# Kernel tuning notes

Hardware: AMD Instinct MI355X
Metric: run time of the kernel (lower is better)

## Reference

```python
import jax, jax.numpy as jnp
import numpy as np

F, N, E = 8, 2048, 32768          # frames, atoms/frame, directed edges/frame
C, NT, NB, NSH = 32, 4, 8, 4      # channels, atom types, Bessel basis, (lmax+1)^2 for lmax=1
R_MAX, L_BOX, NUM_LAYERS = 6.0, 8.0, 3


def setup_inputs() -> dict:
    key = jax.random.key(0)
    ks = jax.random.split(key, 8)
    pos = jax.random.uniform(ks[0], (F, N, 3), jnp.float32) * L_BOX
    src = jax.random.randint(ks[1], (F, 1, E), 0, N)
    off = jax.random.randint(ks[2], (F, 1, E), 1, N)  # avoid self edges
    edge_index = jnp.concatenate([src, (src + off) % N], axis=1).astype(jnp.int32)
    cell = jnp.full((F, 3), L_BOX, jnp.float32)
    atom_types = jax.random.randint(ks[3], (F, N), 0, NT).astype(jnp.int32)
    W_embed = jax.random.normal(ks[4], (NT, C), jnp.float32) * 0.5
    W_rad = jax.random.normal(ks[5], (NUM_LAYERS, NB, C * NSH), jnp.float32) / np.sqrt(NB)
    W_mix = jax.random.normal(ks[6], (NUM_LAYERS, C, C), jnp.float32) / np.sqrt(C)
    w_out = jax.random.normal(ks[7], (C,), jnp.float32) / np.sqrt(C)
    return dict(pos=pos, edge_index=edge_index, cell=cell, atom_types=atom_types,
                W_embed=W_embed, W_rad=W_rad, W_mix=W_mix, w_out=w_out, cut_off=4)


def _atomic_energy(pos_flat, src, dst, shift, at_flat, W_embed, W_rad, W_mix, w_out):
    # edge vectors with (detached) PBC cell shift
    vec = pos_flat[dst] - pos_flat[src] + shift                      # [Et,3]
    r = jnp.sqrt(jnp.sum(vec * vec, -1) + 1e-12)                     # [Et]
    # spherical harmonics lmax=1, component normalization
    Y = jnp.concatenate([jnp.ones_like(r)[:, None],
                         np.sqrt(3.0) * vec / r[:, None]], axis=1)   # [Et,4]
    # Bessel radial basis with p=6 polynomial cutoff envelope
    x = r / R_MAX
    n = jnp.arange(1, NB + 1, dtype=pos_flat.dtype)
    bessel = np.sqrt(2.0 / R_MAX) * jnp.sin(n[None] * np.pi * x[:, None]) / r[:, None]
    env = (1.0 - 28.0 * x**6 + 48.0 * x**7 - 21.0 * x**8) * (x < 1.0).astype(pos_flat.dtype)
    basis = bessel * env[:, None]                                    # [Et,NB]
    FN = pos_flat.shape[0]
    h0 = jax.nn.one_hot(at_flat, NT, dtype=pos_flat.dtype) @ W_embed  # [FN,C]
    feat = jnp.zeros((FN, C, NSH), pos_flat.dtype).at[:, :, 0].set(h0)
    for l in range(NUM_LAYERS):
        R = (basis @ W_rad[l]).reshape(-1, C, NSH)                   # [Et,C,4]
        # gather scalar src feature, tensor-product with SH, radial weight
        msg = R * feat[src, :, 0][:, :, None] * Y[:, None, :]        # [Et,C,4]
        agg = jax.ops.segment_sum(msg, dst, num_segments=FN)         # scatter
        feat = feat + jnp.einsum('ncK,cd->ndK', agg, W_mix[l])       # resnet
    return feat[:, :, 0] @ w_out                                     # [FN]


def reference(pos, edge_index, cell, atom_types, W_embed, W_rad, W_mix, w_out, cut_off):
    Fn, Nn, Ee = pos.shape[0], pos.shape[1], edge_index.shape[2]
    pos_flat = pos.reshape(-1, 3)
    # offset edge indices per frame, flatten frame-major
    ei = (edge_index + (jnp.arange(Fn, dtype=edge_index.dtype) * Nn)[:, None, None])
    ei = ei.transpose(1, 0, 2).reshape(2, -1)
    src, dst = ei[0], ei[1]
    cell_e = jnp.repeat(cell, Ee, axis=0)                            # [F*E,3]
    co = jnp.asarray(cut_off, pos.dtype)
    v = pos_flat[dst] - pos_flat[src]
    shift = jax.lax.stop_gradient(
        cell_e * ((v < -co).astype(pos.dtype) - (v > co).astype(pos.dtype)))
    # symmetrize edges (both directions)
    src2 = jnp.concatenate([src, dst]); dst2 = jnp.concatenate([dst, src])
    shift2 = jnp.concatenate([shift, -shift], axis=0)
    at_flat = atom_types.reshape(-1)
    e_fn = lambda p: _atomic_energy(p, src2, dst2, shift2, at_flat,
                                    W_embed, W_rad, W_mix, w_out)
    atomic_e = e_fn(pos_flat)                                        # [F*N]
    total_energy = atomic_e.reshape(Fn, Nn).sum(axis=1)              # [F]
    force = -jax.grad(lambda p: e_fn(p).sum())(pos_flat)             # -dE/dpos
    return total_energy, force.reshape(Fn, Nn, 3)
```

## Files before the change

kernel.cpp:

```cpp
#include <hip/hip_runtime.h>
#include <math.h>

#define F_NUM 8
#define N_AT 2048
#define E_EDGE 32768
#define FE (F_NUM*E_EDGE)
#define FN (F_NUM*N_AT)
#define CAP 72
#define PI_F 3.14159265358979f

#if defined(__has_builtin)
#if __has_builtin(__builtin_amdgcn_fdot2)
#define HAS_FDOT2 1
#endif
#endif

typedef _Float16 h2 __attribute__((ext_vector_type(2)));

#define XSWZ(bid, G) (((bid) & 7) * ((G) >> 3) + ((bid) >> 3))

__device__ __forceinline__ unsigned short f2b(float x) {
    unsigned int u = __float_as_uint(x);
    u += 0x8000u;
    return (unsigned short)(u >> 16);
}
__device__ __forceinline__ float blo(unsigned int u) { return __uint_as_float(u << 16); }
__device__ __forceinline__ float bhi(unsigned int u) { return __uint_as_float(u & 0xffff0000u); }
__device__ __forceinline__ float b2f(unsigned short u) { return __uint_as_float((unsigned)u << 16); }

__device__ __forceinline__ unsigned f2h(float x) {
    union { _Float16 h; unsigned short u; } cv;
    cv.h = (_Float16)x;
    return (unsigned)cv.u;
}
__device__ __forceinline__ h2 u2h2(unsigned u) {
    union { unsigned u; h2 h; } cv;
    cv.u = u;
    return cv.h;
}
__device__ __forceinline__ float dot8h(uint4 q, const h2* w) {
#ifdef HAS_FDOT2
    float a = __builtin_amdgcn_fdot2(u2h2(q.x), w[0], 0.f, false);
    a = __builtin_amdgcn_fdot2(u2h2(q.y), w[1], a, false);
    a = __builtin_amdgcn_fdot2(u2h2(q.z), w[2], a, false);
    a = __builtin_amdgcn_fdot2(u2h2(q.w), w[3], a, false);
    return a;
#else
    h2 a0 = u2h2(q.x), a1 = u2h2(q.y), a2 = u2h2(q.z), a3 = u2h2(q.w);
    return (float)a0.x*(float)w[0].x + (float)a0.y*(float)w[0].y
         + (float)a1.x*(float)w[1].x + (float)a1.y*(float)w[1].y
         + (float)a2.x*(float)w[2].x + (float)a2.y*(float)w[2].y
         + (float)a3.x*(float)w[3].x + (float)a3.y*(float)w[3].y;
#endif
}
__device__ __forceinline__ void prep_wr(const float* __restrict__ Wrad_l, int c, h2* wr) {
#pragma unroll
    for (int bb = 0; bb < 4; bb++) {
        h2 t;
        t.x = (_Float16)Wrad_l[(2*bb)   * 128 + c * 4];
        t.y = (_Float16)Wrad_l[(2*bb+1) * 128 + c * 4];
        wr[bb] = t;
    }
}

__global__ __launch_bounds__(256) void k_zg(
    int4* __restrict__ cnt4, const float* __restrict__ w_out,
    const float* __restrict__ Wmix2, float* __restrict__ g2)
{
    int bid = blockIdx.x;
    if (bid < 16) {
        cnt4[bid * 256 + threadIdx.x] = make_int4(0, 0, 0, 0);
    } else if (threadIdx.x < 32) {
        int c = threadIdx.x;
        float acc = 0.f;
#pragma unroll
        for (int d = 0; d < 32; d++) acc += w_out[d] * Wmix2[c * 32 + d];
        g2[c] = acc;
    }
}


__global__ __launch_bounds__(256) void k_edges(
    const float* __restrict__ pos, const int* __restrict__ eidx,
    const float* __restrict__ cell, const int* __restrict__ co_p,
    const int* __restrict__ at,
    uint4* __restrict__ dbq, float4* __restrict__ unit, uint2* __restrict__ ab,
    int* __restrict__ cnt, uint4* __restrict__ rec)
{
    int bid = XSWZ(blockIdx.x, FE / 256);
    int k = bid * 256 + threadIdx.x;
    int f = k >> 15;
    int e = k & (E_EDGE - 1);
    int a = eidx[f * 2 * E_EDGE + e] + f * N_AT;
    int b = eidx[f * 2 * E_EDGE + E_EDGE + e] + f * N_AT;
    int ta = at[a], tb = at[b];
    float co = (float)co_p[0];

    float vec[3];
#pragma unroll
    for (int d = 0; d < 3; d++) {
        float v  = pos[3 * b + d] - pos[3 * a + d];
        float cl = cell[3 * f + d];
        float sh = cl * ((v < -co ? 1.f : 0.f) - (v > co ? 1.f : 0.f));
        vec[d] = v + sh;
    }
    float r2   = vec[0]*vec[0] + vec[1]*vec[1] + vec[2]*vec[2] + 1e-12f;
    float r    = sqrtf(r2);
    float rinv = 1.f / r;
    unit[k] = make_float4(vec[0]*rinv, vec[1]*rinv, vec[2]*rinv, 0.f);
    ab[k] = make_uint2((unsigned)((a << 2) | ta), (unsigned)((b << 2) | tb));

    float x = r * (1.f / 6.f);
    float env = 0.f, denv = 0.f;
    if (x < 1.f) {
        float x2 = x*x, x3 = x2*x, x5 = x2*x3, x6 = x5*x, x7 = x6*x, x8 = x7*x;
        env  = 1.f - 28.f*x6 + 48.f*x7 - 21.f*x8;
        denv = -168.f*x5 + 336.f*x6 - 168.f*x7;
    }
    float s1, c1;
    sincosf(PI_F * x, &s1, &c1);
    float sn = s1, cn = c1;
    const float C0 = 0.57735026919f;
    float bs[8], db[8];
#pragma unroll
    for (int n = 1; n <= 8; n++) {
        float kn  = (float)n * PI_F * (1.f / 6.f);
        float bes = C0 * sn * rinv;
        bs[n-1] = bes * env;
        db[n-1] = C0 * rinv * (kn * cn - sn * rinv) * env + bes * denv * (1.f / 6.f);
        float sn2 = sn * c1 + cn * s1;
        float cn2 = cn * c1 - sn * s1;
        sn = sn2; cn = cn2;
    }
    uint4 B, D;
    B.x = f2h(bs[0]) | (f2h(bs[1]) << 16);
    B.y = f2h(bs[2]) | (f2h(bs[3]) << 16);
    B.z = f2h(bs[4]) | (f2h(bs[5]) << 16);
    B.w = f2h(bs[6]) | (f2h(bs[7]) << 16);
    D.x = f2h(db[0]) | (f2h(db[1]) << 16);
    D.y = f2h(db[2]) | (f2h(db[3]) << 16);
    D.z = f2h(db[4]) | (f2h(db[5]) << 16);
    D.w = f2h(db[6]) | (f2h(db[7]) << 16);
    dbq[k] = D;

    int sa = atomicAdd(&cnt[a], 1);
    if (sa < CAP) {
        int ia = 2 * (a * CAP + sa);
        rec[ia]     = make_uint4((unsigned)((b << 3) | tb), B.x, B.y, B.z);
        rec[ia + 1] = make_uint4(B.w, (unsigned)(k << 1), 0, 0);
    }
    int sb = atomicAdd(&cnt[b], 1);
    if (sb < CAP) {
        int ib = 2 * (b * CAP + sb);
        rec[ib]     = make_uint4((unsigned)((a << 3) | 4 | ta), B.x, B.y, B.z);
        rec[ib + 1] = make_uint4(B.w, (unsigned)((k << 1) | 1), 0, 0);
    }
}

#define LOADREC(J, NB, B)                                    \
    {                                                        \
        uint4 ra = rec[2*(J)], rb = rec[2*(J)+1];            \
        NB = (int)ra.x;                                      \
        B  = make_uint4(ra.y, ra.z, ra.w, rb.x);             \
    }

__global__ __launch_bounds__(256, 8) void k_L0(
    const float* __restrict__ W_embed, unsigned short* __restrict__ soq,
    const int* __restrict__ cnt, const uint4* __restrict__ rec,
    const float* __restrict__ Wrad_l, const float* __restrict__ Wmix_l,
    const int* __restrict__ at)
{
    __shared__ float wmix[1024];
    __shared__ float Ash[2][4][32];
    __shared__ float We[128];
    int t = threadIdx.x;
    for (int i = t; i < 1024; i += 256) wmix[i] = Wmix_l[i];
    if (t < 128) We[t] = W_embed[t];
    int bid = XSWZ(blockIdx.x, FN / 2);
    int g = t >> 5, c = t & 31;
    int al = g >> 2, q = g & 3;
    int n = bid * 2 + al;
    h2 wr[4];
    prep_wr(Wrad_l, c, wr);
    __syncthreads();

    int cn = min(cnt[n], CAP);
    int base = n * CAP;
    int j  = base + ((cn * q) >> 2);
    int j1 = base + ((cn * (q + 1)) >> 2);
    float A = 0.f;
    for (; j + 3 < j1; j += 4) {
        int n0, n1, n2, n3;
        uint4 b0, b1, b2, b3;
        LOADREC(j, n0, b0) LOADREC(j+1, n1, b1) LOADREC(j+2, n2, b2) LOADREC(j+3, n3, b3)
        A += dot8h(b0, wr) * We[(n0 & 3) * 32 + c] + dot8h(b1, wr) * We[(n1 & 3) * 32 + c]
           + dot8h(b2, wr) * We[(n2 & 3) * 32 + c] + dot8h(b3, wr) * We[(n3 & 3) * 32 + c];
    }
    for (; j < j1; ++j) {
        int n0; uint4 b0;
        LOADREC(j, n0, b0)
        A += dot8h(b0, wr) * We[(n0 & 3) * 32 + c];
    }
    Ash[al][q][c] = A;
    __syncthreads();
    if (q == 0) {
        float acc = 0.f;
#pragma unroll 8
        for (int cc = 0; cc < 32; cc++) {
            float Av = Ash[al][0][cc] + Ash[al][1][cc] + Ash[al][2][cc] + Ash[al][3][cc];
            acc += Av * wmix[cc * 32 + c];
        }
        soq[n * 32 + c] = f2b(We[at[n] * 32 + c] + acc);
    }
}


__global__ __launch_bounds__(512) void k_L1s(
    const unsigned short* __restrict__ slq, unsigned short* __restrict__ soq,
    const int* __restrict__ cnt, const uint4* __restrict__ rec,
    const float* __restrict__ Wrad_l, const float* __restrict__ Wmix_l)
{
    extern __shared__ unsigned short feat[];
    int t = threadIdx.x;
    int bid = XSWZ(blockIdx.x, 256);
    int frame = bid >> 5;
    int fat = frame * N_AT;
    int abase = fat + (bid & 31) * 64;
    const uint4* src = (const uint4*)(slq + (size_t)fat * 32);
    uint4* dst = (uint4*)feat;
#pragma unroll
    for (int it = 0; it < 16; ++it) dst[t + it * 512] = src[t + it * 512];
    int g = t >> 5, c = t & 31;
    h2 wr[4];
    prep_wr(Wrad_l, c, wr);
    float wv[32];
#pragma unroll
    for (int cc = 0; cc < 32; ++cc) wv[cc] = Wmix_l[cc * 32 + c];
    __syncthreads();

    for (int i = 0; i < 4; ++i) {
        int n = abase + g * 4 + i;
        int cn = min(cnt[n], CAP);
        int j = n * CAP, j1 = n * CAP + cn;
        float A = 0.f;
        for (; j + 3 < j1; j += 4) {
            int n0, n1, n2, n3;
            uint4 b0, b1, b2, b3;
            LOADREC(j, n0, b0) LOADREC(j+1, n1, b1) LOADREC(j+2, n2, b2) LOADREC(j+3, n3, b3)
            float sv0 = b2f(feat[((n0 >> 3) - fat) * 32 + c]);
            float sv1 = b2f(feat[((n1 >> 3) - fat) * 32 + c]);
            float sv2 = b2f(feat[((n2 >> 3) - fat) * 32 + c]);
            float sv3 = b2f(feat[((n3 >> 3) - fat) * 32 + c]);
            A += dot8h(b0, wr) * sv0 + dot8h(b1, wr) * sv1
               + dot8h(b2, wr) * sv2 + dot8h(b3, wr) * sv3;
        }
        for (; j < j1; ++j) {
            int n0; uint4 b0;
            LOADREC(j, n0, b0)
            A += dot8h(b0, wr) * b2f(feat[((n0 >> 3) - fat) * 32 + c]);
        }
        float acc = 0.f;
#pragma unroll
        for (int cc = 0; cc < 32; ++cc) acc += __shfl(A, cc, 32) * wv[cc];
        float base_s = b2f(feat[(n - fat) * 32 + c]);
        soq[n * 32 + c] = f2b(base_s + acc);
    }
}

__global__ __launch_bounds__(512) void k_L2Es(
    const unsigned short* __restrict__ s2q,
    const int* __restrict__ cnt, const uint4* __restrict__ rec,
    const float* __restrict__ Wrad2, const float* __restrict__ Wmix1,
    const float* __restrict__ w_out, const float* __restrict__ g2,
    float* __restrict__ barS2, unsigned short* __restrict__ ba1q, float* __restrict__ epart)
{
    extern __shared__ unsigned short feat[];
    int t = threadIdx.x;
    int bid = XSWZ(blockIdx.x, 256);
    int frame = bid >> 5;
    int fat = frame * N_AT;
    int abase = fat + (bid & 31) * 64;
    const uint4* src = (const uint4*)(s2q + (size_t)fat * 32);
    uint4* dst = (uint4*)feat;
#pragma unroll
    for (int it = 0; it < 16; ++it) dst[t + it * 512] = src[t + it * 512];
    int g = t >> 5, c = t & 31;
    h2 wr[4];
    prep_wr(Wrad2, c, wr);
    float wv[32];
#pragma unroll
    for (int d = 0; d < 32; ++d) wv[d] = Wmix1[c * 32 + d];
    float woc = w_out[c], g2c = g2[c];
    __syncthreads();

    for (int i = 0; i < 4; ++i) {
        int n = abase + g * 4 + i;
        int cn = min(cnt[n], CAP);
        int j = n * CAP, j1 = n * CAP + cn;
        float A = 0.f, S = 0.f;
        for (; j + 3 < j1; j += 4) {
            int n0, n1, n2, n3;
            uint4 b0, b1, b2, b3;
            LOADREC(j, n0, b0) LOADREC(j+1, n1, b1) LOADREC(j+2, n2, b2) LOADREC(j+3, n3, b3)
            float r0 = dot8h(b0, wr), r1 = dot8h(b1, wr), r2 = dot8h(b2, wr), r3 = dot8h(b3, wr);
            A += r0 * b2f(feat[((n0 >> 3) - fat) * 32 + c]) + r1 * b2f(feat[((n1 >> 3) - fat) * 32 + c])
               + r2 * b2f(feat[((n2 >> 3) - fat) * 32 + c]) + r3 * b2f(feat[((n3 >> 3) - fat) * 32 + c]);
            S += r0 + r1 + r2 + r3;
        }
        for (; j < j1; ++j) {
            int n0; uint4 b0;
            LOADREC(j, n0, b0)
            float rr = dot8h(b0, wr);
            A += rr * b2f(feat[((n0 >> 3) - fat) * 32 + c]);
            S += rr;
        }
        float s2n = b2f(feat[(n - fat) * 32 + c]);
        float te = s2n * woc + A * g2c;
#pragma unroll
        for (int o = 1; o <= 16; o <<= 1) te += __shfl_xor(te, o, 32);
        if (c == 0) epart[n] = te;
        float bs2 = woc + g2c * S;
        barS2[n * 32 + c] = bs2;
        float acc = 0.f;
#pragma unroll
        for (int d = 0; d < 32; ++d) acc += __shfl(bs2, d, 32) * wv[d];
        ba1q[n * 32 + c] = f2b(acc);
    }
}

__global__ __launch_bounds__(512) void k_B1Fs(
    const unsigned short* __restrict__ ba1q, const float* __restrict__ barS2,
    const unsigned short* __restrict__ s1q, const unsigned short* __restrict__ s2q,
    const int* __restrict__ cnt, const uint4* __restrict__ rec,
    const float* __restrict__ Wrad1, const float* __restrict__ Wmix0,
    uint2* __restrict__ pk)
{
    extern __shared__ unsigned short feat[];
    int t = threadIdx.x;
    int bid = XSWZ(blockIdx.x, 256);
    int frame = bid >> 5;
    int fat = frame * N_AT;
    int abase = fat + (bid & 31) * 64;
    const uint4* src = (const uint4*)(ba1q + (size_t)fat * 32);
    uint4* dst = (uint4*)feat;
#pragma unroll
    for (int it = 0; it < 16; ++it) dst[t + it * 512] = src[t + it * 512];
    int g = t >> 5, c = t & 31;
    h2 wr[4];
    prep_wr(Wrad1, c, wr);
    float wv[32];
#pragma unroll
    for (int d = 0; d < 32; ++d) wv[d] = Wmix0[c * 32 + d];
    __syncthreads();

    for (int i = 0; i < 4; ++i) {
        int n = abase + g * 4 + i;
        int cn = min(cnt[n], CAP);
        int j = n * CAP, j1 = n * CAP + cn;
        float A = 0.f;
        for (; j + 3 < j1; j += 4) {
            int n0, n1, n2, n3;
            uint4 b0, b1, b2, b3;
            LOADREC(j, n0, b0) LOADREC(j+1, n1, b1) LOADREC(j+2, n2, b2) LOADREC(j+3, n3, b3)
            A += dot8h(b0, wr) * b2f(feat[((n0 >> 3) - fat) * 32 + c])
               + dot8h(b1, wr) * b2f(feat[((n1 >> 3) - fat) * 32 + c])
               + dot8h(b2, wr) * b2f(feat[((n2 >> 3) - fat) * 32 + c])
               + dot8h(b3, wr) * b2f(feat[((n3 >> 3) - fat) * 32 + c]);
        }
        for (; j < j1; ++j) {
            int n0; uint4 b0;
            LOADREC(j, n0, b0)
            A += dot8h(b0, wr) * b2f(feat[((n0 >> 3) - fat) * 32 + c]);
        }
        int n32c = n * 32 + c;
        float bs1 = barS2[n32c] + A;
        float acc = 0.f;
#pragma unroll
        for (int d = 0; d < 32; ++d) acc += __shfl(bs1, d, 32) * wv[d];
        uint2 v;
        v.x = (unsigned)s1q[n32c] | ((unsigned)s2q[n32c] << 16);
        v.y = (unsigned)f2b(acc)  | ((unsigned)feat[(n - fat) * 32 + c] << 16);
        pk[n32c] = v;
    }
}

#define EPG 8
__global__ __launch_bounds__(256, 8) void k_force_e(
    const uint2* __restrict__ pk, const float* __restrict__ g2,
    const uint4* __restrict__ dbq, const uint2* __restrict__ ab,
    const float* __restrict__ W_embed, const float* __restrict__ W_rad,
    float* __restrict__ dEdr)
{
    __shared__ float We[128];
    int t = threadIdx.x;
    if (t < 128) We[t] = W_embed[t];
    int bid = XSWZ(blockIdx.x, FE / (8 * EPG));
    int g = t >> 5;
    int c = t & 31;
    h2 wr0[4], wr1[4], wr2[4];
    prep_wr(W_rad + 0 * 1024, c, wr0);
    prep_wr(W_rad + 1 * 1024, c, wr1);
    prep_wr(W_rad + 2 * 1024, c, wr2);
    float g2c = g2[c];
    __syncthreads();

    int kbase = (bid * 8 + g) * EPG;
    uint2 e2a[EPG];
#pragma unroll
    for (int kk = 0; kk < EPG; ++kk) e2a[kk] = ab[kbase + kk];
#pragma unroll
    for (int kk = 0; kk < EPG; ++kk) {
        int k = kbase + kk;
        uint2 e2 = e2a[kk];
        int a = (int)(e2.x >> 2), b = (int)(e2.y >> 2);
        uint4 d  = dbq[k];
        uint2 qa = pk[a * 32 + c];
        uint2 qb = pk[b * 32 + c];
        float s0a = We[(e2.x & 3) * 32 + c];
        float s0b = We[(e2.y & 3) * 32 + c];
        float dR0 = dot8h(d, wr0), dR1 = dot8h(d, wr1), dR2 = dot8h(d, wr2);
        float tc = dR0 * (blo(qa.y) * s0b + blo(qb.y) * s0a)
                 + dR1 * (bhi(qa.y) * blo(qb.x) + bhi(qb.y) * blo(qa.x))
                 + dR2 * g2c * (bhi(qa.x) + bhi(qb.x));
#pragma unroll
        for (int o = 1; o <= 16; o <<= 1) tc += __shfl_xor(tc, o, 32);
        if (c == 0) dEdr[k] = tc;
    }
}

__global__ __launch_bounds__(256, 8) void k_fgat(
    const int* __restrict__ cnt, const uint4* __restrict__ rec,
    const float* __restrict__ dEdr, const float4* __restrict__ unit,
    const float* __restrict__ epart, float* __restrict__ out)
{
    if (blockIdx.x >= FN / 8) {
        __shared__ float sm[256];
        int f = blockIdx.x - FN / 8, t = threadIdx.x;
        float a = 0.f;
        for (int i = t; i < N_AT; i += 256) a += epart[f * N_AT + i];
        sm[t] = a;
        __syncthreads();
        for (int s = 128; s; s >>= 1) {
            if (t < s) sm[t] += sm[t + s];
            __syncthreads();
        }
        if (t == 0) out[f] = sm[0];
        return;
    }
    int t = threadIdx.x;
    int bid = XSWZ(blockIdx.x, FN / 8);
    int g = t >> 5, lane = t & 31;
    int n = bid * 8 + g;
    int cn = min(cnt[n], CAP);
    int base = n * CAP;
    float Fx = 0.f, Fy = 0.f, Fz = 0.f;
    for (int j = base + lane; j < base + cn; j += 32) {
        unsigned s = rec[2 * j + 1].y;
        int k = (int)(s >> 1);
        float sg = (s & 1) ? -1.f : 1.f;
        float4 uv = unit[k];
        float d = dEdr[k] * sg;
        Fx += d * uv.x; Fy += d * uv.y; Fz += d * uv.z;
    }
#pragma unroll
    for (int o = 1; o <= 16; o <<= 1) {
        Fx += __shfl_xor(Fx, o, 32);
        Fy += __shfl_xor(Fy, o, 32);
        Fz += __shfl_xor(Fz, o, 32);
    }
    if (lane == 0) {
        out[8 + n * 3 + 0] = Fx;
        out[8 + n * 3 + 1] = Fy;
        out[8 + n * 3 + 2] = Fz;
    }
}

extern "C" void kernel_launch(void* const* d_in, const int* in_sizes, int n_in,
                              void* d_out, int out_size, void* d_ws, size_t ws_size,
                              hipStream_t stream)
{
    const float* pos     = (const float*)d_in[0];
    const int*   eidx    = (const int*)  d_in[1];
    const float* cell    = (const float*)d_in[2];
    const int*   at      = (const int*)  d_in[3];
    const float* W_embed = (const float*)d_in[4];
    const float* W_rad   = (const float*)d_in[5];
    const float* W_mix   = (const float*)d_in[6];
    const float* w_out   = (const float*)d_in[7];
    const int*   co      = (const int*)  d_in[8];

    char* p = (char*)d_ws;
    auto carve = [&](size_t bytes) -> char* {
        char* r = p;
        p += (bytes + 255) & ~(size_t)255;
        return r;
    };
    uint4*          dbq    = (uint4*)          carve((size_t)FE * 16);
    float4*         unit   = (float4*)         carve((size_t)FE * 16);
    uint2*          ab     = (uint2*)          carve((size_t)FE * 8);
    unsigned short* s1q    = (unsigned short*) carve((size_t)FN * 32 * 2);
    unsigned short* s2q    = (unsigned short*) carve((size_t)FN * 32 * 2);
    unsigned short* ba1q   = (unsigned short*) carve((size_t)FN * 32 * 2);
    float*          barS2  = (float*)          carve((size_t)FN * 32 * 4);
    uint2*          pk     = (uint2*)          carve((size_t)FN * 32 * 8);
    float*          g2     = (float*)          carve(32 * 4);
    float*          epart  = (float*)          carve((size_t)FN * 4);
    float*          dEdr   = (float*)          carve((size_t)FE * 4);
    int*            cnt    = (int*)            carve((size_t)FN * 4);
    uint4*          rec    = (uint4*)          carve((size_t)FN * CAP * 32);

    const size_t SMEM = (size_t)N_AT * 32 * 2;

    k_zg<<<17, 256, 0, stream>>>((int4*)cnt, w_out, W_mix + 2 * 1024, g2);

    k_edges<<<FE / 256, 256, 0, stream>>>(pos, eidx, cell, co, at, dbq, unit, ab, cnt, rec);

    k_L0<<<FN / 2, 256, 0, stream>>>(W_embed, s1q, cnt, rec,
                                     W_rad + 0 * 1024, W_mix + 0 * 1024, at);
    k_L1s<<<256, 512, SMEM, stream>>>(s1q, s2q, cnt, rec,
                                      W_rad + 1 * 1024, W_mix + 1 * 1024);
    k_L2Es<<<256, 512, SMEM, stream>>>(s2q, cnt, rec, W_rad + 2 * 1024,
                                       W_mix + 1 * 1024, w_out, g2, barS2, ba1q, epart);
    k_B1Fs<<<256, 512, SMEM, stream>>>(ba1q, barS2, s1q, s2q, cnt, rec,
                                       W_rad + 1 * 1024, W_mix + 0 * 1024, pk);
    k_force_e<<<FE / (8 * EPG), 256, 0, stream>>>(pk, g2, dbq, ab, W_embed, W_rad, dEdr);
    k_fgat<<<FN / 8 + F_NUM, 256, 0, stream>>>(cnt, rec, dEdr, unit, epart, (float*)d_out);
}
```

Before: 184.6 us.

## Restructure L0 per-warp atoms, prefetch force loads, precompute edge force vectors

k_L0 now assigns four whole atoms to each 32-lane group in 512-thread blocks and mixes channels with warp shuffles against register-held W_mix, replacing the shared-memory partial sums and the block barrier. k_force_e issues all gather loads for its eight edges before doing any arithmetic, to raise memory-level parallelism, and its occupancy hint is lowered to make room for the extra registers. It also multiplies dE/dr by the unit vector and stores a float4 force per edge, so k_fgat reads one array instead of two. In exchange the edge output grows from a scalar to a float4, and L0 gets less parallelism per atom.

```diff
diff --git a/kernel.cpp b/kernel.cpp
--- a/kernel.cpp
+++ b/kernel.cpp
@@ -164,52 +164,45 @@
         B  = make_uint4(ra.y, ra.z, ra.w, rb.x);             \
     }
 
-__global__ __launch_bounds__(256, 8) void k_L0(
+__global__ __launch_bounds__(512) void k_L0(
     const float* __restrict__ W_embed, unsigned short* __restrict__ soq,
     const int* __restrict__ cnt, const uint4* __restrict__ rec,
     const float* __restrict__ Wrad_l, const float* __restrict__ Wmix_l,
     const int* __restrict__ at)
 {
-    __shared__ float wmix[1024];
-    __shared__ float Ash[2][4][32];
     __shared__ float We[128];
     int t = threadIdx.x;
-    for (int i = t; i < 1024; i += 256) wmix[i] = Wmix_l[i];
     if (t < 128) We[t] = W_embed[t];
-    int bid = XSWZ(blockIdx.x, FN / 2);
+    int bid = XSWZ(blockIdx.x, FN / 64);
     int g = t >> 5, c = t & 31;
-    int al = g >> 2, q = g & 3;
-    int n = bid * 2 + al;
+    int abase = bid * 64;
     h2 wr[4];
     prep_wr(Wrad_l, c, wr);
+    float wv[32];
+#pragma unroll
+    for (int cc = 0; cc < 32; ++cc) wv[cc] = Wmix_l[cc * 32 + c];
     __syncthreads();
 
-    int cn = min(cnt[n], CAP);
-    int base = n * CAP;
-    int j  = base + ((cn * q) >> 2);
-    int j1 = base + ((cn * (q + 1)) >> 2);
-    float A = 0.f;
-    for (; j + 3 < j1; j += 4) {
-        int n0, n1, n2, n3;
-        uint4 b0, b1, b2, b3;
-        LOADREC(j, n0, b0) LOADREC(j+1, n1, b1) LOADREC(j+2, n2, b2) LOADREC(j+3, n3, b3)
-        A += dot8h(b0, wr) * We[(n0 & 3) * 32 + c] + dot8h(b1, wr) * We[(n1 & 3) * 32 + c]
-           + dot8h(b2, wr) * We[(n2 & 3) * 32 + c] + dot8h(b3, wr) * We[(n3 & 3) * 32 + c];
-    }
-    for (; j < j1; ++j) {
-        int n0; uint4 b0;
-        LOADREC(j, n0, b0)
-        A += dot8h(b0, wr) * We[(n0 & 3) * 32 + c];
-    }
-    Ash[al][q][c] = A;
-    __syncthreads();
-    if (q == 0) {
+    for (int i = 0; i < 4; ++i) {
+        int n = abase + g * 4 + i;
+        int cn = min(cnt[n], CAP);
+        int j = n * CAP, j1 = n * CAP + cn;
+        float A = 0.f;
+        for (; j + 3 < j1; j += 4) {
+            int n0, n1, n2, n3;
+            uint4 b0, b1, b2, b3;
+            LOADREC(j, n0, b0) LOADREC(j+1, n1, b1) LOADREC(j+2, n2, b2) LOADREC(j+3, n3, b3)
+            A += dot8h(b0, wr) * We[(n0 & 3) * 32 + c] + dot8h(b1, wr) * We[(n1 & 3) * 32 + c]
+               + dot8h(b2, wr) * We[(n2 & 3) * 32 + c] + dot8h(b3, wr) * We[(n3 & 3) * 32 + c];
+        }
+        for (; j < j1; ++j) {
+            int n0; uint4 b0;
+            LOADREC(j, n0, b0)
+            A += dot8h(b0, wr) * We[(n0 & 3) * 32 + c];
+        }
         float acc = 0.f;
-#pragma unroll 8
-        for (int cc = 0; cc < 32; cc++) {
-            float Av = Ash[al][0][cc] + Ash[al][1][cc] + Ash[al][2][cc] + Ash[al][3][cc];
-            acc += Av * wmix[cc * 32 + c];
-        }
+#pragma unroll
+        for (int cc = 0; cc < 32; ++cc) acc += __shfl(A, cc, 32) * wv[cc];
         soq[n * 32 + c] = f2b(We[at[n] * 32 + c] + acc);
     }
 }
@@ -385,11 +378,12 @@
 }
 
 #define EPG 8
-__global__ __launch_bounds__(256, 8) void k_force_e(
+__global__ __launch_bounds__(256, 4) void k_force_e(
     const uint2* __restrict__ pk, const float* __restrict__ g2,
     const uint4* __restrict__ dbq, const uint2* __restrict__ ab,
+    const float4* __restrict__ unit,
     const float* __restrict__ W_embed, const float* __restrict__ W_rad,
-    float* __restrict__ dEdr)
+    float4* __restrict__ fvec)
 {
     __shared__ float We[128];
     int t = threadIdx.x;
@@ -408,29 +402,36 @@
     uint2 e2a[EPG];
 #pragma unroll
     for (int kk = 0; kk < EPG; ++kk) e2a[kk] = ab[kbase + kk];
+    uint2 qa[EPG], qb[EPG];
+    uint4 dd[EPG];
+#pragma unroll
+    for (int kk = 0; kk < EPG; ++kk) {
+        qa[kk] = pk[(e2a[kk].x >> 2) * 32 + c];
+        qb[kk] = pk[(e2a[kk].y >> 2) * 32 + c];
+        dd[kk] = dbq[kbase + kk];
+    }
 #pragma unroll
     for (int kk = 0; kk < EPG; ++kk) {
         int k = kbase + kk;
         uint2 e2 = e2a[kk];
-        int a = (int)(e2.x >> 2), b = (int)(e2.y >> 2);
-        uint4 d  = dbq[k];
-        uint2 qa = pk[a * 32 + c];
-        uint2 qb = pk[b * 32 + c];
         float s0a = We[(e2.x & 3) * 32 + c];
         float s0b = We[(e2.y & 3) * 32 + c];
-        float dR0 = dot8h(d, wr0), dR1 = dot8h(d, wr1), dR2 = dot8h(d, wr2);
-        float tc = dR0 * (blo(qa.y) * s0b + blo(qb.y) * s0a)
-                 + dR1 * (bhi(qa.y) * blo(qb.x) + bhi(qb.y) * blo(qa.x))
-                 + dR2 * g2c * (bhi(qa.x) + bhi(qb.x));
+        float dR0 = dot8h(dd[kk], wr0), dR1 = dot8h(dd[kk], wr1), dR2 = dot8h(dd[kk], wr2);
+        float tc = dR0 * (blo(qa[kk].y) * s0b + blo(qb[kk].y) * s0a)
+                 + dR1 * (bhi(qa[kk].y) * blo(qb[kk].x) + bhi(qb[kk].y) * blo(qa[kk].x))
+                 + dR2 * g2c * (bhi(qa[kk].x) + bhi(qb[kk].x));
 #pragma unroll
         for (int o = 1; o <= 16; o <<= 1) tc += __shfl_xor(tc, o, 32);
-        if (c == 0) dEdr[k] = tc;
+        if (c < 4) {
+            float uval = ((const float*)unit)[4 * k + c];
+            ((float*)fvec)[4 * k + c] = tc * uval;
+        }
     }
 }
 
 __global__ __launch_bounds__(256, 8) void k_fgat(
     const int* __restrict__ cnt, const uint4* __restrict__ rec,
-    const float* __restrict__ dEdr, const float4* __restrict__ unit,
+    const float4* __restrict__ fvec,
     const float* __restrict__ epart, float* __restrict__ out)
 {
     if (blockIdx.x >= FN / 8) {
@@ -458,9 +459,8 @@
         unsigned s = rec[2 * j + 1].y;
         int k = (int)(s >> 1);
         float sg = (s & 1) ? -1.f : 1.f;
-        float4 uv = unit[k];
-        float d = dEdr[k] * sg;
-        Fx += d * uv.x; Fy += d * uv.y; Fz += d * uv.z;
+        float4 fv = fvec[k];
+        Fx += sg * fv.x; Fy += sg * fv.y; Fz += sg * fv.z;
     }
 #pragma unroll
     for (int o = 1; o <= 16; o <<= 1) {
@@ -497,6 +497,7 @@
     };
     uint4*          dbq    = (uint4*)          carve((size_t)FE * 16);
     float4*         unit   = (float4*)         carve((size_t)FE * 16);
+    float4*         fvec   = (float4*)         carve((size_t)FE * 16);
     uint2*          ab     = (uint2*)          carve((size_t)FE * 8);
     unsigned short* s1q    = (unsigned short*) carve((size_t)FN * 32 * 2);
     unsigned short* s2q    = (unsigned short*) carve((size_t)FN * 32 * 2);
@@ -505,7 +506,6 @@
     uint2*          pk     = (uint2*)          carve((size_t)FN * 32 * 8);
     float*          g2     = (float*)          carve(32 * 4);
     float*          epart  = (float*)          carve((size_t)FN * 4);
-    float*          dEdr   = (float*)          carve((size_t)FE * 4);
     int*            cnt    = (int*)            carve((size_t)FN * 4);
     uint4*          rec    = (uint4*)          carve((size_t)FN * CAP * 32);
 
@@ -515,14 +515,14 @@
 
     k_edges<<<FE / 256, 256, 0, stream>>>(pos, eidx, cell, co, at, dbq, unit, ab, cnt, rec);
 
-    k_L0<<<FN / 2, 256, 0, stream>>>(W_embed, s1q, cnt, rec,
-                                     W_rad + 0 * 1024, W_mix + 0 * 1024, at);
+    k_L0<<<FN / 64, 512, 0, stream>>>(W_embed, s1q, cnt, rec,
+                                      W_rad + 0 * 1024, W_mix + 0 * 1024, at);
     k_L1s<<<256, 512, SMEM, stream>>>(s1q, s2q, cnt, rec,
                                       W_rad + 1 * 1024, W_mix + 1 * 1024);
     k_L2Es<<<256, 512, SMEM, stream>>>(s2q, cnt, rec, W_rad + 2 * 1024,
                                        W_mix + 1 * 1024, w_out, g2, barS2, ba1q, epart);
     k_B1Fs<<<256, 512, SMEM, stream>>>(ba1q, barS2, s1q, s2q, cnt, rec,
                                        W_rad + 1 * 1024, W_mix + 0 * 1024, pk);
-    k_force_e<<<FE / (8 * EPG), 256, 0, stream>>>(pk, g2, dbq, ab, W_embed, W_rad, dEdr);
-    k_fgat<<<FN / 8 + F_NUM, 256, 0, stream>>>(cnt, rec, dEdr, unit, epart, (float*)d_out);
-}
+    k_force_e<<<FE / (8 * EPG), 256, 0, stream>>>(pk, g2, dbq, ab, unit, W_embed, W_rad, fvec);
+    k_fgat<<<FN / 8 + F_NUM, 256, 0, stream>>>(cnt, rec, fvec, epart, (float*)d_out);
+}
```

New measurement: 179.3 us. 1.03x faster.
